# Kernel tuning notes

Measured on AMD Instinct MI355X. Metric: run time of the kernel, lower is better.

Reference implementation:

```python
import jax, jax.numpy as jnp
import numpy as np

B, N, D, H = 4, 2048, 1024, 16
DH = D // H


def setup_inputs() -> dict:
    key = jax.random.key(0)
    k_x, k_q, k_k, k_v, k_o = jax.random.split(key, 5)
    s = 1.0 / np.sqrt(D)
    return {
        "x": jax.random.normal(k_x, (B, N, D), dtype=jnp.float32),
        "mask": jnp.ones((B, N), dtype=bool),
        "Wq": jax.random.normal(k_q, (D, D), dtype=jnp.float32) * s,
        "Wk": jax.random.normal(k_k, (D, D), dtype=jnp.float32) * s,
        "Wv": jax.random.normal(k_v, (D, D), dtype=jnp.float32) * s,
        "Wo": jax.random.normal(k_o, (D, D), dtype=jnp.float32) * s,
    }


def reference(x, mask, Wq, Wk, Wv, Wo):
    # nn.Linear(bias=False): y = x @ W.T ; weights stored [out, in]
    q = jnp.einsum("bnd,ed->bne", x, Wq)
    k = jnp.einsum("bnd,ed->bne", x, Wk)
    v = jnp.einsum("bnd,ed->bne", x, Wv)
    # split heads: [b, n, d] -> [b, h, n, dh]
    def split(t):
        return t.reshape(B, N, H, DH).transpose(0, 2, 1, 3)
    q, k, v = split(q), split(k), split(v)
    # naive scaled dot-product attention (mask is dead code in the source)
    scores = jnp.einsum("bhnd,bhmd->bhnm", q, k) / jnp.sqrt(jnp.float32(DH))
    attn = jax.nn.softmax(scores, axis=-1)
    out = jnp.einsum("bhnm,bhmd->bhnd", attn, v)  # [b, h, n, dh]
    # merge heads: [b, h, n, dh] -> [b, n, d]
    out = out.transpose(0, 2, 1, 3).reshape(B, N, D)
    return jnp.einsum("bnd,ed->bne", out, Wo)
```

## Files before the change

### kernel.cpp

```cpp
#include <hip/hip_runtime.h>
#include <math.h>

constexpr int Bc  = 4;
constexpr int Nc  = 2048;
constexpr int Dc  = 1024;
constexpr int Hc  = 16;
constexpr int DHc = 64;
constexpr int Mrows = Bc * Nc;

typedef unsigned short ushortT;
typedef __attribute__((ext_vector_type(8))) short bf16x8;
typedef __attribute__((ext_vector_type(8))) unsigned short u16x8;
typedef __attribute__((ext_vector_type(4))) unsigned short u16x4;
typedef __attribute__((ext_vector_type(4))) float f32x4;

#define QSCALE 0.18033688011112043f

#define GLD_LDS16(g, l)                                                        \
  __builtin_amdgcn_global_load_lds(                                            \
      (const __attribute__((address_space(1))) void*)(g),                      \
      (__attribute__((address_space(3))) void*)(l), 16, 0, 0)

__device__ inline ushortT f2bf(float f) {
  unsigned int u = __float_as_uint(f);
  u += 0x7fffu + ((u >> 16) & 1u);
  return (ushortT)(u >> 16);
}

__device__ inline float fexp2(float x) { return __builtin_amdgcn_exp2f(x); }

__global__ __launch_bounds__(256) void cvt_kernel(
    const float* __restrict__ x, const float* __restrict__ wq,
    const float* __restrict__ wk, const float* __restrict__ wv,
    const float* __restrict__ wo, ushortT* __restrict__ dst) {
  const int g = blockIdx.x * 256 + threadIdx.x;
  const float* src;
  size_t soff, doff;
  if (g < 2097152) {
    src = x;
    soff = (size_t)g * 4;
    doff = soff;
  } else {
    const int t = g - 2097152;
    const int w = t >> 18;
    const int off = t & 262143;
    src = (w == 0) ? wq : (w == 1) ? wk : (w == 2) ? wv : wo;
    soff = (size_t)off * 4;
    doff = 8388608u + (size_t)w * 1048576u + (size_t)off * 4;
  }
  float4 v = *(const float4*)(src + soff);
  ushort4 o = make_ushort4(f2bf(v.x), f2bf(v.y), f2bf(v.z), f2bf(v.w));
  *(ushort4*)(dst + doff) = o;
}

template <int QKV>
__global__ __launch_bounds__(256) void mfma_gemm(const ushortT* __restrict__ A,
                                                 const ushortT* __restrict__ W0,
                                                 void* __restrict__ C0) {
  __shared__ ushortT As[128 * 32];
  __shared__ ushortT Bs[128 * 32];

  const int tid = threadIdx.x;
  const int wave = tid >> 6, lane = tid & 63;
  const int quad = lane >> 4, lrow = lane & 15;
  const int bx = blockIdx.x, by = blockIdx.y;
  const int wsel = QKV ? (bx >> 3) : 0;
  const int e0 = QKV ? ((bx & 7) * 128) : (bx * 128);
  const int m0 = by * 128;
  const ushortT* Wp = W0 + (size_t)wsel * (Dc * Dc);
  const float oscale = (QKV && wsel == 0) ? QSCALE : 1.0f;

  const ushortT* ag = A  + (size_t)(m0 + wave * 32 + (lane >> 2)) * Dc + (lane & 3) * 8;
  const ushortT* bg = Wp + (size_t)(e0 + wave * 32 + (lane >> 2)) * Dc + (lane & 3) * 8;
  ushortT* al = As + wave * 1024 + lane * 8;
  ushortT* bl = Bs + wave * 1024 + lane * 8;

  f32x4 acc[4][4];
#pragma unroll
  for (int i = 0; i < 4; ++i)
#pragma unroll
    for (int j = 0; j < 4; ++j) acc[i][j] = (f32x4){0.f, 0.f, 0.f, 0.f};

  const int wm = (wave >> 1) * 64, wn = (wave & 1) * 64;

  for (int k0 = 0; k0 < Dc; k0 += 32) {
    __syncthreads();
    GLD_LDS16(ag, al);
    GLD_LDS16(ag + 16 * Dc, al + 512);
    GLD_LDS16(bg, bl);
    GLD_LDS16(bg + 16 * Dc, bl + 512);
    ag += 32;
    bg += 32;
    __syncthreads();

    bf16x8 af[4], bf[4];
#pragma unroll
    for (int mt = 0; mt < 4; ++mt)
      af[mt] = *(const bf16x8*)(As + (wm + mt * 16 + lrow) * 32 + quad * 8);
#pragma unroll
    for (int nt = 0; nt < 4; ++nt)
      bf[nt] = *(const bf16x8*)(Bs + (wn + nt * 16 + lrow) * 32 + quad * 8);
#pragma unroll
    for (int mt = 0; mt < 4; ++mt)
#pragma unroll
      for (int nt = 0; nt < 4; ++nt)
        acc[mt][nt] = __builtin_amdgcn_mfma_f32_16x16x32_bf16(
            af[mt], bf[nt], acc[mt][nt], 0, 0, 0);
  }

#pragma unroll
  for (int mt = 0; mt < 4; ++mt) {
#pragma unroll
    for (int nt = 0; nt < 4; ++nt) {
#pragma unroll
      for (int r = 0; r < 4; ++r) {
        const int m = m0 + wm + mt * 16 + quad * 4 + r;
        const int e = e0 + wn + nt * 16 + lrow;
        const float v = acc[mt][nt][r] * oscale;
        if (QKV) {
          const int b = m >> 11, n = m & 2047;
          const int h = e >> 6, dh = e & 63;
          ushortT* C = (ushortT*)C0 + (size_t)wsel * ((size_t)Mrows * Dc);
          C[(((size_t)(b * Hc + h)) * Nc + n) * DHc + dh] = f2bf(v);
        } else {
          ((float*)C0)[(size_t)m * Dc + e] = v;
        }
      }
    }
  }
}

__global__ __launch_bounds__(256, 2) void attn_mfma(const ushortT* __restrict__ Q,
                                                    const ushortT* __restrict__ K,
                                                    const ushortT* __restrict__ V,
                                                    ushortT* __restrict__ O) {
  __shared__ ushortT smemA[256 * 72];
  __shared__ ushortT Ks[2 * 64 * 32];
  __shared__ ushortT Vt[64 * 72];

  const int tid = threadIdx.x;
  const int wave = tid >> 6, lane = tid & 63;
  const int quad = lane >> 4, lrow = lane & 15;
  const int bh = blockIdx.y;
  const int q0 = blockIdx.x * 256;

  const ushortT* qg = Q + (size_t)bh * Nc * DHc;
  const ushortT* kg = K + (size_t)bh * Nc * DHc;
  const ushortT* vg = V + (size_t)bh * Nc * DHc;

#pragma unroll
  for (int c = 0; c < 2; ++c)
#pragma unroll
    for (int rh = 0; rh < 4; ++rh) {
      const int row = wave * 64 + rh * 16;
      GLD_LDS16(qg + (size_t)(q0 + row + (lane >> 2)) * DHc + c * 32 + (lane & 3) * 8,
                smemA + (c * 256 + row) * 32 + lane * 8);
    }
  __syncthreads();

  bf16x8 af_q[4][2];
#pragma unroll
  for (int mt = 0; mt < 4; ++mt)
#pragma unroll
    for (int ks = 0; ks < 2; ++ks)
      af_q[mt][ks] = *(const bf16x8*)(smemA +
          ((ks * 256 + wave * 64 + mt * 16 + lrow) * 32 + quad * 8));
  __syncthreads();

  f32x4 o_acc[4][4];
#pragma unroll
  for (int mt = 0; mt < 4; ++mt)
#pragma unroll
    for (int nt = 0; nt < 4; ++nt) o_acc[mt][nt] = (f32x4){0.f, 0.f, 0.f, 0.f};
  float l_i[16];
#pragma unroll
  for (int i = 0; i < 16; ++i) l_i[i] = 0.f;

  const int kq = tid & 15;
  const int dhg = (tid >> 4) * 4;

  for (int k0 = 0; k0 < Nc; k0 += 64) {
    __syncthreads();

#pragma unroll
    for (int i = 0; i < 2; ++i) {
      const int cid = wave * 2 + i;
      const int c = cid & 1, kb = (cid >> 1) * 16;
      GLD_LDS16(kg + (size_t)(k0 + kb + (lane >> 2)) * DHc + c * 32 + (lane & 3) * 8,
                Ks + (c * 64 + kb) * 32 + lane * 8);
    }

    {
      ushortT tmp[4][4];
#pragma unroll
      for (int g = 0; g < 4; ++g) {
        const u16x4 v = *(const u16x4*)(vg + (size_t)(k0 + kq + 16 * g) * DHc + dhg);
#pragma unroll
        for (int d = 0; d < 4; ++d) tmp[d][g] = v[d];
      }
#pragma unroll
      for (int d = 0; d < 4; ++d)
        *(u16x4*)(Vt + (dhg + d) * 72 + kq * 4) = *(const u16x4*)tmp[d];
    }
    __syncthreads();

    bf16x8 bf_k[4][2];
#pragma unroll
    for (int nt = 0; nt < 4; ++nt)
#pragma unroll
      for (int ks = 0; ks < 2; ++ks)
        bf_k[nt][ks] = *(const bf16x8*)(Ks + (ks * 64 + nt * 16 + lrow) * 32 + quad * 8);

    f32x4 s_acc[4][4];
#pragma unroll
    for (int mt = 0; mt < 4; ++mt)
#pragma unroll
      for (int nt = 0; nt < 4; ++nt) {
        s_acc[mt][nt] = (f32x4){0.f, 0.f, 0.f, 0.f};
#pragma unroll
        for (int ks = 0; ks < 2; ++ks)
          s_acc[mt][nt] = __builtin_amdgcn_mfma_f32_16x16x32_bf16(
              af_q[mt][ks], bf_k[nt][ks], s_acc[mt][nt], 0, 0, 0);
      }

#pragma unroll
    for (int mt = 0; mt < 4; ++mt) {
#pragma unroll
      for (int r = 0; r < 4; ++r) {
        const float p0 = fexp2(s_acc[mt][0][r]);
        const float p1 = fexp2(s_acc[mt][1][r]);
        const float p2 = fexp2(s_acc[mt][2][r]);
        const float p3 = fexp2(s_acc[mt][3][r]);
        l_i[mt * 4 + r] += (p0 + p1) + (p2 + p3);
        const unsigned pk01 = __builtin_amdgcn_perm(
            __float_as_uint(p1), __float_as_uint(p0), 0x07060302u);
        const unsigned pk23 = __builtin_amdgcn_perm(
            __float_as_uint(p3), __float_as_uint(p2), 0x07060302u);
        const int row = wave * 64 + mt * 16 + quad * 4 + r;
        *(uint2*)(smemA + row * 72 + lrow * 4) = make_uint2(pk01, pk23);
      }
    }
    asm volatile("s_waitcnt lgkmcnt(0)" ::: "memory");

    bf16x8 af_p[4][2], bf_v[4][2];
#pragma unroll
    for (int mt = 0; mt < 4; ++mt)
#pragma unroll
      for (int ks = 0; ks < 2; ++ks)
        af_p[mt][ks] = *(const bf16x8*)(smemA +
            (wave * 64 + mt * 16 + lrow) * 72 + ks * 32 + quad * 8);
#pragma unroll
    for (int nt = 0; nt < 4; ++nt)
#pragma unroll
      for (int ks = 0; ks < 2; ++ks)
        bf_v[nt][ks] = *(const bf16x8*)(Vt + (nt * 16 + lrow) * 72 + ks * 32 + quad * 8);
#pragma unroll
    for (int mt = 0; mt < 4; ++mt)
#pragma unroll
      for (int nt = 0; nt < 4; ++nt)
#pragma unroll
        for (int ks = 0; ks < 2; ++ks)
          o_acc[mt][nt] = __builtin_amdgcn_mfma_f32_16x16x32_bf16(
              af_p[mt][ks], bf_v[nt][ks], o_acc[mt][nt], 0, 0, 0);
  }

#pragma unroll
  for (int i = 0; i < 16; ++i) {
    float s = l_i[i];
#pragma unroll
    for (int off = 8; off >= 1; off >>= 1) s += __shfl_xor(s, off, 16);
    l_i[i] = s;
  }

  const int b = bh / Hc, h = bh % Hc;
#pragma unroll
  for (int mt = 0; mt < 4; ++mt) {
#pragma unroll
    for (int r = 0; r < 4; ++r) {
      const float inv_l = 1.0f / l_i[mt * 4 + r];
      const int n = q0 + wave * 64 + mt * 16 + quad * 4 + r;
      const size_t base = ((size_t)b * Nc + n) * Dc + h * DHc;
#pragma unroll
      for (int nt = 0; nt < 4; ++nt)
        O[base + nt * 16 + lrow] = f2bf(o_acc[mt][nt][r] * inv_l);
    }
  }
}

extern "C" void kernel_launch(void* const* d_in, const int* in_sizes, int n_in,
                              void* d_out, int out_size, void* d_ws,
                              size_t ws_size, hipStream_t stream) {
  const float* x  = (const float*)d_in[0];
  const float* Wq = (const float*)d_in[2];
  const float* Wk = (const float*)d_in[3];
  const float* Wv = (const float*)d_in[4];
  const float* Wo = (const float*)d_in[5];

  ushortT* ws16 = (ushortT*)d_ws;
  ushortT* xb   = ws16;
  ushortT* wqb  = xb + (size_t)Mrows * Dc;
  ushortT* qkvb = wqb + 4 * (size_t)Dc * Dc;
  ushortT* qb   = qkvb;
  ushortT* kb   = qb + (size_t)Mrows * Dc;
  ushortT* vb   = kb + (size_t)Mrows * Dc;
  ushortT* aob  = vb + (size_t)Mrows * Dc;
  ushortT* wob  = wqb + 3 * (size_t)Dc * Dc;

  dim3 blk(256);
  hipLaunchKernelGGL(cvt_kernel, dim3(12288), blk, 0, stream, x, Wq, Wk, Wv, Wo,
                     ws16);

  hipLaunchKernelGGL((mfma_gemm<1>), dim3(24, Mrows / 128), blk, 0, stream, xb,
                     wqb, (void*)qkvb);

  hipLaunchKernelGGL(attn_mfma, dim3(Nc / 256, Bc * Hc), blk, 0, stream, qb,
                     kb, vb, aob);

  hipLaunchKernelGGL((mfma_gemm<0>), dim3(8, Mrows / 128), blk, 0, stream, aob,
                     wob, d_out);
}
```

Measured before the change: 283.2 us.

## Double-buffer K/V tiles and halve attention query tile to raise occupancy

The attention kernel now prefetches the next K tile (async global-to-LDS) and V tile (into registers, transposed into a second LDS buffer) while computing the current tile, with one barrier per iteration instead of two. The query tile per block shrinks from 256 to 128 rows, which doubles the grid to 1024 blocks and raises the occupancy hint from 2 to 3 blocks per CU. The smaller per-wave tile halves Q and accumulator register use, but each K/V tile is now reused by fewer query rows, so total K/V loads double.

New measurement: 301.3 us. 6.4% more time.

```diff
diff --git a/kernel.cpp b/kernel.cpp
--- a/kernel.cpp
+++ b/kernel.cpp
@@ -130,90 +130,105 @@
   }
 }
 
-__global__ __launch_bounds__(256, 2) void attn_mfma(const ushortT* __restrict__ Q,
+__global__ __launch_bounds__(256, 3) void attn_mfma(const ushortT* __restrict__ Q,
                                                     const ushortT* __restrict__ K,
                                                     const ushortT* __restrict__ V,
                                                     ushortT* __restrict__ O) {
-  __shared__ ushortT smemA[256 * 72];
-  __shared__ ushortT Ks[2 * 64 * 32];
-  __shared__ ushortT Vt[64 * 72];
+  __shared__ ushortT smemA[128 * 72];
+  __shared__ ushortT Ks[2][64 * 64];
+  __shared__ ushortT Vt[2][64 * 68];
 
   const int tid = threadIdx.x;
   const int wave = tid >> 6, lane = tid & 63;
   const int quad = lane >> 4, lrow = lane & 15;
   const int bh = blockIdx.y;
-  const int q0 = blockIdx.x * 256;
+  const int q0 = blockIdx.x * 128;
 
   const ushortT* qg = Q + (size_t)bh * Nc * DHc;
   const ushortT* kg = K + (size_t)bh * Nc * DHc;
   const ushortT* vg = V + (size_t)bh * Nc * DHc;
 
+  const int kq = tid & 15;
+  const int dhg = (tid >> 4) * 4;
+
 #pragma unroll
   for (int c = 0; c < 2; ++c)
 #pragma unroll
-    for (int rh = 0; rh < 4; ++rh) {
-      const int row = wave * 64 + rh * 16;
+    for (int i = 0; i < 2; ++i) {
+      const int row = wave * 32 + i * 16;
       GLD_LDS16(qg + (size_t)(q0 + row + (lane >> 2)) * DHc + c * 32 + (lane & 3) * 8,
-                smemA + (c * 256 + row) * 32 + lane * 8);
-    }
+                smemA + (c * 128 + row) * 32 + lane * 8);
+    }
+#pragma unroll
+  for (int i = 0; i < 2; ++i) {
+    const int cid = wave * 2 + i;
+    const int c = cid & 1, kb = (cid >> 1) * 16;
+    GLD_LDS16(kg + (size_t)(kb + (lane >> 2)) * DHc + c * 32 + (lane & 3) * 8,
+              &Ks[0][(c * 64 + kb) * 32 + lane * 8]);
+  }
+  u16x4 vreg[4];
+#pragma unroll
+  for (int g = 0; g < 4; ++g)
+    vreg[g] = *(const u16x4*)(vg + (size_t)(kq + 16 * g) * DHc + dhg);
+
   __syncthreads();
 
-  bf16x8 af_q[4][2];
-#pragma unroll
-  for (int mt = 0; mt < 4; ++mt)
+  bf16x8 af_q[2][2];
+#pragma unroll
+  for (int mt = 0; mt < 2; ++mt)
 #pragma unroll
     for (int ks = 0; ks < 2; ++ks)
       af_q[mt][ks] = *(const bf16x8*)(smemA +
-          ((ks * 256 + wave * 64 + mt * 16 + lrow) * 32 + quad * 8));
+          ((ks * 128 + wave * 32 + mt * 16 + lrow) * 32 + quad * 8));
+
+  {
+    ushortT tmp[4][4];
+#pragma unroll
+    for (int g = 0; g < 4; ++g)
+#pragma unroll
+      for (int d = 0; d < 4; ++d) tmp[d][g] = vreg[g][d];
+#pragma unroll
+    for (int d = 0; d < 4; ++d)
+      *(u16x4*)(&Vt[0][(dhg + d) * 68 + kq * 4]) = *(const u16x4*)tmp[d];
+  }
   __syncthreads();
 
-  f32x4 o_acc[4][4];
-#pragma unroll
-  for (int mt = 0; mt < 4; ++mt)
+  f32x4 o_acc[2][4];
+#pragma unroll
+  for (int mt = 0; mt < 2; ++mt)
 #pragma unroll
     for (int nt = 0; nt < 4; ++nt) o_acc[mt][nt] = (f32x4){0.f, 0.f, 0.f, 0.f};
-  float l_i[16];
-#pragma unroll
-  for (int i = 0; i < 16; ++i) l_i[i] = 0.f;
-
-  const int kq = tid & 15;
-  const int dhg = (tid >> 4) * 4;
+  float l_i[8];
+#pragma unroll
+  for (int i = 0; i < 8; ++i) l_i[i] = 0.f;
 
   for (int k0 = 0; k0 < Nc; k0 += 64) {
-    __syncthreads();
-
-#pragma unroll
-    for (int i = 0; i < 2; ++i) {
-      const int cid = wave * 2 + i;
-      const int c = cid & 1, kb = (cid >> 1) * 16;
-      GLD_LDS16(kg + (size_t)(k0 + kb + (lane >> 2)) * DHc + c * 32 + (lane & 3) * 8,
-                Ks + (c * 64 + kb) * 32 + lane * 8);
-    }
-
-    {
-      ushortT tmp[4][4];
-#pragma unroll
-      for (int g = 0; g < 4; ++g) {
-        const u16x4 v = *(const u16x4*)(vg + (size_t)(k0 + kq + 16 * g) * DHc + dhg);
-#pragma unroll
-        for (int d = 0; d < 4; ++d) tmp[d][g] = v[d];
+    const int cur = (k0 >> 6) & 1, nxt = cur ^ 1;
+    const bool pref = (k0 + 64 < Nc);
+
+    if (pref) {
+#pragma unroll
+      for (int i = 0; i < 2; ++i) {
+        const int cid = wave * 2 + i;
+        const int c = cid & 1, kb = (cid >> 1) * 16;
+        GLD_LDS16(kg + (size_t)(k0 + 64 + kb + (lane >> 2)) * DHc + c * 32 + (lane & 3) * 8,
+                  &Ks[nxt][(c * 64 + kb) * 32 + lane * 8]);
       }
 #pragma unroll
-      for (int d = 0; d < 4; ++d)
-        *(u16x4*)(Vt + (dhg + d) * 72 + kq * 4) = *(const u16x4*)tmp[d];
-    }
-    __syncthreads();
+      for (int g = 0; g < 4; ++g)
+        vreg[g] = *(const u16x4*)(vg + (size_t)(k0 + 64 + kq + 16 * g) * DHc + dhg);
+    }
 
     bf16x8 bf_k[4][2];
 #pragma unroll
     for (int nt = 0; nt < 4; ++nt)
 #pragma unroll
       for (int ks = 0; ks < 2; ++ks)
-        bf_k[nt][ks] = *(const bf16x8*)(Ks + (ks * 64 + nt * 16 + lrow) * 32 + quad * 8);
-
-    f32x4 s_acc[4][4];
-#pragma unroll
-    for (int mt = 0; mt < 4; ++mt)
+        bf_k[nt][ks] = *(const bf16x8*)(&Ks[cur][(ks * 64 + nt * 16 + lrow) * 32 + quad * 8]);
+
+    f32x4 s_acc[2][4];
+#pragma unroll
+    for (int mt = 0; mt < 2; ++mt)
 #pragma unroll
       for (int nt = 0; nt < 4; ++nt) {
         s_acc[mt][nt] = (f32x4){0.f, 0.f, 0.f, 0.f};
@@ -223,8 +238,19 @@
               af_q[mt][ks], bf_k[nt][ks], s_acc[mt][nt], 0, 0, 0);
       }
 
-#pragma unroll
-    for (int mt = 0; mt < 4; ++mt) {
+    if (pref) {
+      ushortT tmp[4][4];
+#pragma unroll
+      for (int g = 0; g < 4; ++g)
+#pragma unroll
+        for (int d = 0; d < 4; ++d) tmp[d][g] = vreg[g][d];
+#pragma unroll
+      for (int d = 0; d < 4; ++d)
+        *(u16x4*)(&Vt[nxt][(dhg + d) * 68 + kq * 4]) = *(const u16x4*)tmp[d];
+    }
+
+#pragma unroll
+    for (int mt = 0; mt < 2; ++mt) {
 #pragma unroll
       for (int r = 0; r < 4; ++r) {
         const float p0 = fexp2(s_acc[mt][0][r]);
@@ -236,36 +262,38 @@
             __float_as_uint(p1), __float_as_uint(p0), 0x07060302u);
         const unsigned pk23 = __builtin_amdgcn_perm(
             __float_as_uint(p3), __float_as_uint(p2), 0x07060302u);
-        const int row = wave * 64 + mt * 16 + quad * 4 + r;
+        const int row = wave * 32 + mt * 16 + quad * 4 + r;
         *(uint2*)(smemA + row * 72 + lrow * 4) = make_uint2(pk01, pk23);
       }
     }
     asm volatile("s_waitcnt lgkmcnt(0)" ::: "memory");
 
-    bf16x8 af_p[4][2], bf_v[4][2];
-#pragma unroll
-    for (int mt = 0; mt < 4; ++mt)
+    bf16x8 af_p[2][2], bf_v[4][2];
+#pragma unroll
+    for (int mt = 0; mt < 2; ++mt)
 #pragma unroll
       for (int ks = 0; ks < 2; ++ks)
         af_p[mt][ks] = *(const bf16x8*)(smemA +
-            (wave * 64 + mt * 16 + lrow) * 72 + ks * 32 + quad * 8);
+            (wave * 32 + mt * 16 + lrow) * 72 + ks * 32 + quad * 8);
 #pragma unroll
     for (int nt = 0; nt < 4; ++nt)
 #pragma unroll
       for (int ks = 0; ks < 2; ++ks)
-        bf_v[nt][ks] = *(const bf16x8*)(Vt + (nt * 16 + lrow) * 72 + ks * 32 + quad * 8);
-#pragma unroll
-    for (int mt = 0; mt < 4; ++mt)
+        bf_v[nt][ks] = *(const bf16x8*)(&Vt[cur][(nt * 16 + lrow) * 68 + ks * 32 + quad * 8]);
+#pragma unroll
+    for (int mt = 0; mt < 2; ++mt)
 #pragma unroll
       for (int nt = 0; nt < 4; ++nt)
 #pragma unroll
         for (int ks = 0; ks < 2; ++ks)
           o_acc[mt][nt] = __builtin_amdgcn_mfma_f32_16x16x32_bf16(
               af_p[mt][ks], bf_v[nt][ks], o_acc[mt][nt], 0, 0, 0);
-  }
-
-#pragma unroll
-  for (int i = 0; i < 16; ++i) {
+
+    __syncthreads();
+  }
+
+#pragma unroll
+  for (int i = 0; i < 8; ++i) {
     float s = l_i[i];
 #pragma unroll
     for (int off = 8; off >= 1; off >>= 1) s += __shfl_xor(s, off, 16);
@@ -274,11 +302,11 @@
 
   const int b = bh / Hc, h = bh % Hc;
 #pragma unroll
-  for (int mt = 0; mt < 4; ++mt) {
+  for (int mt = 0; mt < 2; ++mt) {
 #pragma unroll
     for (int r = 0; r < 4; ++r) {
       const float inv_l = 1.0f / l_i[mt * 4 + r];
-      const int n = q0 + wave * 64 + mt * 16 + quad * 4 + r;
+      const int n = q0 + wave * 32 + mt * 16 + quad * 4 + r;
       const size_t base = ((size_t)b * Nc + n) * Dc + h * DHc;
 #pragma unroll
       for (int nt = 0; nt < 4; ++nt)
@@ -313,7 +341,7 @@
   hipLaunchKernelGGL((mfma_gemm<1>), dim3(24, Mrows / 128), blk, 0, stream, xb,
                      wqb, (void*)qkvb);
 
-  hipLaunchKernelGGL(attn_mfma, dim3(Nc / 256, Bc * Hc), blk, 0, stream, qb,
+  hipLaunchKernelGGL(attn_mfma, dim3(Nc / 128, Bc * Hc), blk, 0, stream, qb,
                      kb, vb, aob);
 
   hipLaunchKernelGGL((mfma_gemm<0>), dim3(8, Mrows / 128), blk, 0, stream, aob,
```

## Double-buffer K/V tiles in attention and deepen GEMM K-step to 64

Applied to the files above, without the earlier changes.

In the attention kernel, the next K tile is prefetched into a second LDS buffer with async global-to-LDS loads, and the next V tile is loaded into registers before the current tile's QK^T and PV work. The registers are transposed into Vt after the PV MFMAs, so global-load latency overlaps compute. In the projection GEMM, each loop iteration now loads two 32-wide K slices, halving the number of barrier pairs per tile. The cost is more LDS use, which may reduce occupancy, and extra registers held across the loop body.

Measured after the change: 281.7 us. About the same (-0.5%).

```diff
diff --git a/kernel.cpp b/kernel.cpp
--- a/kernel.cpp
+++ b/kernel.cpp
@@ -10,7 +10,6 @@
 
 typedef unsigned short ushortT;
 typedef __attribute__((ext_vector_type(8))) short bf16x8;
-typedef __attribute__((ext_vector_type(8))) unsigned short u16x8;
 typedef __attribute__((ext_vector_type(4))) unsigned short u16x4;
 typedef __attribute__((ext_vector_type(4))) float f32x4;
 
@@ -57,8 +56,8 @@
 __global__ __launch_bounds__(256) void mfma_gemm(const ushortT* __restrict__ A,
                                                  const ushortT* __restrict__ W0,
                                                  void* __restrict__ C0) {
-  __shared__ ushortT As[128 * 32];
-  __shared__ ushortT Bs[128 * 32];
+  __shared__ ushortT As[2][128 * 32];
+  __shared__ ushortT Bs[2][128 * 32];
 
   const int tid = threadIdx.x;
   const int wave = tid >> 6, lane = tid & 63;
@@ -72,8 +71,7 @@
 
   const ushortT* ag = A  + (size_t)(m0 + wave * 32 + (lane >> 2)) * Dc + (lane & 3) * 8;
   const ushortT* bg = Wp + (size_t)(e0 + wave * 32 + (lane >> 2)) * Dc + (lane & 3) * 8;
-  ushortT* al = As + wave * 1024 + lane * 8;
-  ushortT* bl = Bs + wave * 1024 + lane * 8;
+  const int lbase = wave * 1024 + lane * 8;
 
   f32x4 acc[4][4];
 #pragma unroll
@@ -83,29 +81,35 @@
 
   const int wm = (wave >> 1) * 64, wn = (wave & 1) * 64;
 
-  for (int k0 = 0; k0 < Dc; k0 += 32) {
+  for (int k0 = 0; k0 < Dc; k0 += 64) {
     __syncthreads();
-    GLD_LDS16(ag, al);
-    GLD_LDS16(ag + 16 * Dc, al + 512);
-    GLD_LDS16(bg, bl);
-    GLD_LDS16(bg + 16 * Dc, bl + 512);
-    ag += 32;
-    bg += 32;
+#pragma unroll
+    for (int p = 0; p < 2; ++p) {
+      GLD_LDS16(ag + p * 32, &As[p][lbase]);
+      GLD_LDS16(ag + p * 32 + 16 * Dc, &As[p][lbase + 512]);
+      GLD_LDS16(bg + p * 32, &Bs[p][lbase]);
+      GLD_LDS16(bg + p * 32 + 16 * Dc, &Bs[p][lbase + 512]);
+    }
+    ag += 64;
+    bg += 64;
     __syncthreads();
 
-    bf16x8 af[4], bf[4];
-#pragma unroll
-    for (int mt = 0; mt < 4; ++mt)
-      af[mt] = *(const bf16x8*)(As + (wm + mt * 16 + lrow) * 32 + quad * 8);
-#pragma unroll
-    for (int nt = 0; nt < 4; ++nt)
-      bf[nt] = *(const bf16x8*)(Bs + (wn + nt * 16 + lrow) * 32 + quad * 8);
-#pragma unroll
-    for (int mt = 0; mt < 4; ++mt)
+#pragma unroll
+    for (int p = 0; p < 2; ++p) {
+      bf16x8 af[4], bf[4];
+#pragma unroll
+      for (int mt = 0; mt < 4; ++mt)
+        af[mt] = *(const bf16x8*)(&As[p][(wm + mt * 16 + lrow) * 32 + quad * 8]);
 #pragma unroll
       for (int nt = 0; nt < 4; ++nt)
-        acc[mt][nt] = __builtin_amdgcn_mfma_f32_16x16x32_bf16(
-            af[mt], bf[nt], acc[mt][nt], 0, 0, 0);
+        bf[nt] = *(const bf16x8*)(&Bs[p][(wn + nt * 16 + lrow) * 32 + quad * 8]);
+#pragma unroll
+      for (int mt = 0; mt < 4; ++mt)
+#pragma unroll
+        for (int nt = 0; nt < 4; ++nt)
+          acc[mt][nt] = __builtin_amdgcn_mfma_f32_16x16x32_bf16(
+              af[mt], bf[nt], acc[mt][nt], 0, 0, 0);
+    }
   }
 
 #pragma unroll
@@ -135,7 +139,7 @@
                                                     const ushortT* __restrict__ V,
                                                     ushortT* __restrict__ O) {
   __shared__ ushortT smemA[256 * 72];
-  __shared__ ushortT Ks[2 * 64 * 32];
+  __shared__ ushortT Ks[2][64 * 64];
   __shared__ ushortT Vt[64 * 72];
 
   const int tid = threadIdx.x;
@@ -148,6 +152,9 @@
   const ushortT* kg = K + (size_t)bh * Nc * DHc;
   const ushortT* vg = V + (size_t)bh * Nc * DHc;
 
+  const int kq = tid & 15;
+  const int dhg = (tid >> 4) * 4;
+
 #pragma unroll
   for (int c = 0; c < 2; ++c)
 #pragma unroll
@@ -156,6 +163,18 @@
       GLD_LDS16(qg + (size_t)(q0 + row + (lane >> 2)) * DHc + c * 32 + (lane & 3) * 8,
                 smemA + (c * 256 + row) * 32 + lane * 8);
     }
+#pragma unroll
+  for (int i = 0; i < 2; ++i) {
+    const int cid = wave * 2 + i;
+    const int c = cid & 1, kb = (cid >> 1) * 16;
+    GLD_LDS16(kg + (size_t)(kb + (lane >> 2)) * DHc + c * 32 + (lane & 3) * 8,
+              &Ks[0][(c * 64 + kb) * 32 + lane * 8]);
+  }
+  u16x4 vreg[4];
+#pragma unroll
+  for (int g = 0; g < 4; ++g)
+    vreg[g] = *(const u16x4*)(vg + (size_t)(kq + 16 * g) * DHc + dhg);
+
   __syncthreads();
 
   bf16x8 af_q[4][2];
@@ -165,6 +184,17 @@
     for (int ks = 0; ks < 2; ++ks)
       af_q[mt][ks] = *(const bf16x8*)(smemA +
           ((ks * 256 + wave * 64 + mt * 16 + lrow) * 32 + quad * 8));
+
+  {
+    ushortT tmp[4][4];
+#pragma unroll
+    for (int g = 0; g < 4; ++g)
+#pragma unroll
+      for (int d = 0; d < 4; ++d) tmp[d][g] = vreg[g][d];
+#pragma unroll
+    for (int d = 0; d < 4; ++d)
+      *(u16x4*)(Vt + (dhg + d) * 72 + kq * 4) = *(const u16x4*)tmp[d];
+  }
   __syncthreads();
 
   f32x4 o_acc[4][4];
@@ -176,40 +206,29 @@
 #pragma unroll
   for (int i = 0; i < 16; ++i) l_i[i] = 0.f;
 
-  const int kq = tid & 15;
-  const int dhg = (tid >> 4) * 4;
-
   for (int k0 = 0; k0 < Nc; k0 += 64) {
-    __syncthreads();
-
-#pragma unroll
-    for (int i = 0; i < 2; ++i) {
-      const int cid = wave * 2 + i;
-      const int c = cid & 1, kb = (cid >> 1) * 16;
-      GLD_LDS16(kg + (size_t)(k0 + kb + (lane >> 2)) * DHc + c * 32 + (lane & 3) * 8,
-                Ks + (c * 64 + kb) * 32 + lane * 8);
-    }
-
-    {
-      ushortT tmp[4][4];
-#pragma unroll
-      for (int g = 0; g < 4; ++g) {
-        const u16x4 v = *(const u16x4*)(vg + (size_t)(k0 + kq + 16 * g) * DHc + dhg);
-#pragma unroll
-        for (int d = 0; d < 4; ++d) tmp[d][g] = v[d];
+    const int cur = (k0 >> 6) & 1, nxt = cur ^ 1;
+    const bool pref = (k0 + 64 < Nc);
+
+    if (pref) {
+#pragma unroll
+      for (int i = 0; i < 2; ++i) {
+        const int cid = wave * 2 + i;
+        const int c = cid & 1, kb = (cid >> 1) * 16;
+        GLD_LDS16(kg + (size_t)(k0 + 64 + kb + (lane >> 2)) * DHc + c * 32 + (lane & 3) * 8,
+                  &Ks[nxt][(c * 64 + kb) * 32 + lane * 8]);
       }
 #pragma unroll
-      for (int d = 0; d < 4; ++d)
-        *(u16x4*)(Vt + (dhg + d) * 72 + kq * 4) = *(const u16x4*)tmp[d];
-    }
-    __syncthreads();
+      for (int g = 0; g < 4; ++g)
+        vreg[g] = *(const u16x4*)(vg + (size_t)(k0 + 64 + kq + 16 * g) * DHc + dhg);
+    }
 
     bf16x8 bf_k[4][2];
 #pragma unroll
     for (int nt = 0; nt < 4; ++nt)
 #pragma unroll
       for (int ks = 0; ks < 2; ++ks)
-        bf_k[nt][ks] = *(const bf16x8*)(Ks + (ks * 64 + nt * 16 + lrow) * 32 + quad * 8);
+        bf_k[nt][ks] = *(const bf16x8*)(&Ks[cur][(ks * 64 + nt * 16 + lrow) * 32 + quad * 8]);
 
     f32x4 s_acc[4][4];
 #pragma unroll
@@ -262,6 +281,21 @@
         for (int ks = 0; ks < 2; ++ks)
           o_acc[mt][nt] = __builtin_amdgcn_mfma_f32_16x16x32_bf16(
               af_p[mt][ks], bf_v[nt][ks], o_acc[mt][nt], 0, 0, 0);
+
+    __syncthreads();
+
+    if (pref) {
+      ushortT tmp[4][4];
+#pragma unroll
+      for (int g = 0; g < 4; ++g)
+#pragma unroll
+        for (int d = 0; d < 4; ++d) tmp[d][g] = vreg[g][d];
+#pragma unroll
+      for (int d = 0; d < 4; ++d)
+        *(u16x4*)(Vt + (dhg + d) * 72 + kq * 4) = *(const u16x4*)tmp[d];
+    }
+
+    __syncthreads();
   }
 
 #pragma unroll
```
